# Kernel optimization log

Measured on AMD Instinct MI355X. Metric: run time of the kernel, lower is better.

Reference implementation:

```python
import jax, jax.numpy as jnp
import numpy as np

N = 50000       # nodes
E = 800000      # edges (avg degree 16)
IN_DIM = 64
H = 64          # hidden_dim
OUT_DIM = 64
R = 8           # n_relations
L = 3           # n_layers
LN_EPS = 1e-5
NEG_SLOPE = 0.2


def _layer_norm(x, g, b):
    mu = jnp.mean(x, axis=-1, keepdims=True)
    var = jnp.mean((x - mu) ** 2, axis=-1, keepdims=True)
    return (x - mu) * jax.lax.rsqrt(var + LN_EPS) * g + b


def setup_inputs() -> dict:
    key = jax.random.key(0)
    ks = jax.random.split(key, 10)
    s = 0.05
    return {
        "x": jax.random.normal(ks[0], (N, IN_DIM), jnp.float32),
        "edge_index": jax.random.randint(ks[1], (2, E), 0, N),
        "edge_type": jax.random.randint(ks[2], (E,), 0, R),
        "W_in": jax.random.normal(ks[3], (H, IN_DIM), jnp.float32) * s,
        "b_in": jnp.zeros((H,), jnp.float32),
        "W_rel": jax.random.normal(ks[4], (R, H, H), jnp.float32) * s,   # no bias
        "W_gate": jax.random.normal(ks[5], (R, H, H), jnp.float32) * s,
        "b_gate": jnp.zeros((R, H), jnp.float32),
        "W_att": jax.random.normal(ks[6], (R, 2 * H), jnp.float32) * s,  # Linear(2H,1) per relation
        "b_att": jnp.zeros((R,), jnp.float32),
        "ln_gamma": jnp.ones((L, H), jnp.float32),
        "ln_beta": jnp.zeros((L, H), jnp.float32),
        "W_out": jax.random.normal(ks[7], (OUT_DIM, H), jnp.float32) * s,
        "b_out": jnp.zeros((OUT_DIM,), jnp.float32),
    }


def reference(x, edge_index, edge_type, W_in, b_in, W_rel, W_gate, b_gate,
              W_att, b_att, ln_gamma, ln_beta, W_out, b_out):
    src, dst = edge_index[0], edge_index[1]
    Wa_src, Wa_dst = W_att[:, :H], W_att[:, H:]      # [R,H] each
    seg = dst * R + edge_type                        # combined (node, relation) scatter key
    eidx = jnp.arange(E)

    h = jax.nn.relu(x @ W_in.T + b_in)               # [N,H]

    for layer in range(L):
        h_src = h[src]                               # [E,H] gather
        h_dst = h[dst]                               # [E,H] gather
        # attention score of each edge under its own relation's Linear(2H,1)
        scores_all = h_src @ Wa_src.T + h_dst @ Wa_dst.T + b_att   # [E,R]
        scores = scores_all[eidx, edge_type]                        # [E]
        scores = jax.nn.leaky_relu(scores, NEG_SLOPE)
        # softmax over dim=0 within each relation's edge set (as in the torch code)
        m = jax.ops.segment_max(scores, edge_type, num_segments=R)
        ex = jnp.exp(scores - m[edge_type])
        denom = jax.ops.segment_sum(ex, edge_type, num_segments=R)
        att = ex / denom[edge_type]                                 # [E]
        # relation-specific linear of source features (linear commutes with gather)
        hWr = jnp.einsum('nh,rkh->nrk', h, W_rel)                   # [N,R,H]
        msg = hWr[src, edge_type] * att[:, None]                    # [E,H]
        # per-relation scatter-add into destinations
        agg = jax.ops.segment_sum(msg, seg, num_segments=N * R)     # [N*R,H]
        agg = agg.reshape(N, R, H)
        gate = jax.nn.sigmoid(jnp.einsum('nh,rkh->nrk', h, W_gate) + b_gate)  # [N,R,H]
        h_new = jnp.mean(gate * agg, axis=1)         # sum(messages)/n_relations
        h = jax.nn.relu(_layer_norm(h + h_new, ln_gamma[layer], ln_beta[layer]))

    return h @ W_out.T + b_out
```

## Files before the change

kernel.cpp:

```cpp
#include <hip/hip_runtime.h>
#include <math.h>

#define NN 50000
#define EE 800000
#define HH 64
#define RR 8
#define LL 3
#define NR (NN * RR)
#define NB ((NR + 255) / 256)
#define LN_EPS 1e-5f
#define NEG_SLOPE 0.2f
#define LDH 68
#define OTB (16 * LDH)
#define DSPREAD 64

typedef __attribute__((ext_vector_type(8))) short bf8;
typedef __attribute__((ext_vector_type(4))) float f4;
typedef __attribute__((ext_vector_type(2))) float f2;
typedef __attribute__((ext_vector_type(8))) unsigned short us8;
typedef __attribute__((ext_vector_type(2))) unsigned int u2;
typedef __attribute__((ext_vector_type(4))) unsigned int u4;

#define PIN(x) asm volatile("" :: "v"(x))

#define WLOADP(d0, d1, sbase, vbyte) \
    asm volatile("global_load_dwordx4 %0, %2, %3 offset:0\n\t" \
                 "global_load_dwordx4 %1, %2, %3 offset:64" \
        : "=&v"(d0), "=&v"(d1) : "v"(vbyte), "s"(sbase) : "memory")
#define WWAIT4() do { asm volatile("s_waitcnt vmcnt(4)" ::: "memory"); \
    __builtin_amdgcn_sched_barrier(0); } while (0)
#define WWAIT0() do { asm volatile("s_waitcnt vmcnt(0)" ::: "memory"); \
    __builtin_amdgcn_sched_barrier(0); } while (0)

__device__ __forceinline__ unsigned short bf16r(float f) {
    unsigned u = __float_as_uint(f);
    unsigned r = u + 0x7fffu + ((u >> 16) & 1u);
    return (unsigned short)(r >> 16);
}
__device__ __forceinline__ float bf2f(unsigned short u) {
    return __uint_as_float(((unsigned)u) << 16);
}
__device__ __forceinline__ bf8 asbf8(u4 v) {
    union { u4 a; bf8 b; } c; c.a = v; return c.b;
}
__device__ __forceinline__ void stage16(const void* g, void* l) {
    __builtin_amdgcn_global_load_lds(
        (const __attribute__((address_space(1))) void*)g,
        (__attribute__((address_space(3))) void*)l, 16, 0, 0);
}

__global__ __launch_bounds__(256) void proj_in(
    const float* __restrict__ x, const float* __restrict__ W,
    const float* __restrict__ bias, const unsigned short* __restrict__ WaB,
    float* __restrict__ h, unsigned short* __restrict__ hbf,
    float* __restrict__ s_src, float* __restrict__ s_dst) {
    __shared__ float WT[64 * LDH];
    __shared__ float xs[16 * LDH];
    __shared__ float hs[16 * LDH];
    int tid = threadIdx.x;
    int n0 = blockIdx.x * 16;
    #pragma unroll
    for (int s = 0; s < 16; ++s) {
        int idx = tid + 256 * s;
        int k = idx >> 6, i = idx & 63;
        WT[i * LDH + k] = W[idx];
    }
    int row = tid >> 4, cg = tid & 15;
    {
        f4 v = ((const f4*)x)[(size_t)(n0 + row) * 16 + cg];
        *(f4*)&xs[row * LDH + cg * 4] = v;
    }
    __syncthreads();
    f4 acc;
    {
        f4 b = *(const f4*)(bias + cg * 4);
        acc = b;
        #pragma unroll
        for (int i = 0; i < 64; ++i) {
            float xv = xs[row * LDH + i];
            f4 wt = *(const f4*)&WT[i * LDH + cg * 4];
            acc[0] += xv * wt[0];
            acc[1] += xv * wt[1];
            acc[2] += xv * wt[2];
            acc[3] += xv * wt[3];
        }
        #pragma unroll
        for (int j = 0; j < 4; ++j) acc[j] = fmaxf(acc[j], 0.f);
        int n = n0 + row;
        *(f4*)(h + (size_t)n * 64 + cg * 4) = acc;
        u2 u;
        u[0] = (unsigned)bf16r(acc[0]) | ((unsigned)bf16r(acc[1]) << 16);
        u[1] = (unsigned)bf16r(acc[2]) | ((unsigned)bf16r(acc[3]) << 16);
        *(u2*)(hbf + (size_t)n * 64 + cg * 4) = u;
        *(f4*)&hs[row * LDH + cg * 4] = acc;
    }
    __syncthreads();
    if (tid < 64) {
        int lane = tid;
        int quad = lane >> 4, lr = lane & 15;
        f4 sc = (f4){0.f, 0.f, 0.f, 0.f};
        #pragma unroll
        for (int kb = 0; kb < 2; ++kb) {
            const float* p = &hs[lr * LDH + kb * 32 + quad * 8];
            bf8 a;
            #pragma unroll
            for (int j = 0; j < 8; ++j) a[j] = (short)bf16r(p[j]);
            const bf8* bw = (const bf8*)(WaB + lr * 64 + kb * 32 + quad * 8);
            sc = __builtin_amdgcn_mfma_f32_16x16x32_bf16(a, *bw, sc, 0, 0, 0);
        }
        #pragma unroll
        for (int j = 0; j < 4; ++j) {
            int n = n0 + quad * 4 + j;
            if (lr < 8) s_src[n * 8 + lr] = sc[j];
            else        s_dst[n * 8 + (lr - 8)] = sc[j];
        }
    }
}

__global__ void edge_count(const int* __restrict__ ei, const int* __restrict__ et,
                           int* __restrict__ counts, int* __restrict__ rank) {
    int e = blockIdx.x * 256 + threadIdx.x;
    int d = ei[EE + e], t = et[e];
    rank[e] = atomicAdd(&counts[d * 8 + t], 1);
}

__global__ void scan1(const int* __restrict__ counts, int* __restrict__ offs,
                      int* __restrict__ bsum) {
    __shared__ int s[256];
    int tid = threadIdx.x;
    int i = blockIdx.x * 256 + tid;
    int v = (i < NR) ? counts[i] : 0;
    s[tid] = v; __syncthreads();
    for (int d = 1; d < 256; d <<= 1) {
        int x = (tid >= d) ? s[tid - d] : 0;
        __syncthreads();
        s[tid] += x;
        __syncthreads();
    }
    if (i < NR) offs[i] = s[tid] - v;
    if (tid == 255) bsum[blockIdx.x] = s[255];
}

__global__ void scan2(int* __restrict__ bsum) {
    __shared__ int s[1024];
    int tid = threadIdx.x;
    int carry = 0;
    for (int c0 = 0; c0 < NB; c0 += 1024) {
        int i = c0 + tid;
        int v = (i < NB) ? bsum[i] : 0;
        s[tid] = v; __syncthreads();
        for (int d = 1; d < 1024; d <<= 1) {
            int x = (tid >= d) ? s[tid - d] : 0;
            __syncthreads();
            s[tid] += x;
            __syncthreads();
        }
        if (i < NB) bsum[i] = carry + s[tid] - v;
        int tot = s[1023];
        __syncthreads();
        carry += tot;
    }
}

__global__ void edge_fill(const int* __restrict__ ei, const int* __restrict__ et,
                          const int* __restrict__ rank, const int* __restrict__ offs,
                          const int* __restrict__ bsum, u2* __restrict__ spack) {
    int e = blockIdx.x * 256 + threadIdx.x;
    int s = ei[e], d = ei[EE + e], t = et[e];
    int seg = d * 8 + t;
    int slot = offs[seg] + bsum[seg >> 8] + rank[e];
    spack[slot] = (u2){(unsigned)s, (unsigned)seg};
}

__global__ void cvt_w(const float* __restrict__ Wr, const float* __restrict__ Wg,
                      const float* __restrict__ Wa, const float* __restrict__ Wo,
                      unsigned short* __restrict__ WrB, unsigned short* __restrict__ WgB,
                      unsigned short* __restrict__ WaB, unsigned short* __restrict__ WoB) {
    int i = blockIdx.x * 256 + threadIdx.x;
    WrB[i] = bf16r(Wr[i]);
    WgB[i] = bf16r(Wg[i]);
    if (i < 1024) {
        int row = i >> 6, k = i & 63;
        float v = (row < 8) ? Wa[row * 128 + k] : Wa[(row - 8) * 128 + 64 + k];
        WaB[i] = bf16r(v);
    }
    if (i < 4096) WoB[i] = bf16r(Wo[i]);
}

__global__ void edge_softmax2(const u2* __restrict__ spack,
                              const float* __restrict__ s_src, const float* __restrict__ s_dst,
                              const float* __restrict__ b_att,
                              u2* __restrict__ epack, float* __restrict__ dpart) {
    __shared__ float lsum[4][8];
    int tid = threadIdx.x;
    if (tid < 32) lsum[tid >> 3][tid & 7] = 0.f;
    __syncthreads();
    int slot = blockIdx.x * 256 + tid;
    u2 sp = spack[slot];
    int src = (int)sp[0];
    int seg = (int)sp[1];
    int t = seg & 7;
    float sc = s_src[src * 8 + t] + s_dst[seg] + b_att[t];
    sc = (sc >= 0.f) ? sc : NEG_SLOPE * sc;
    float ex = __expf(sc);
    epack[slot] = (u2){(unsigned)src, __float_as_uint(ex)};
    atomicAdd(&lsum[tid >> 6][t], ex);
    __syncthreads();
    if (tid < 8) {
        float v = lsum[0][tid] + lsum[1][tid] + lsum[2][tid] + lsum[3][tid];
        atomicAdd(&dpart[(blockIdx.x & (DSPREAD - 1)) * 16 + tid], v);
    }
}

__global__ void denom_reduce(const float* __restrict__ dpartL,
                             float* __restrict__ idn8L) {
    __shared__ float sb[256];
    int t = threadIdx.x;
    int rb = t >> 3, ty = t & 7;
    float v = dpartL[rb * 16 + ty] + dpartL[(rb + 32) * 16 + ty];
    sb[t] = v; __syncthreads();
    for (int st = 128; st >= 8; st >>= 1) {
        if (t < st) sb[t] += sb[t + st];
        __syncthreads();
    }
    if (t < 8) idn8L[t] = 1.f / sb[t];
}

__global__ __launch_bounds__(256, 4) void gather_seg(
    const int* __restrict__ offs, const int* __restrict__ bsum,
    const u2* __restrict__ epack, const float* __restrict__ idn8L,
    const unsigned short* __restrict__ hbf_in,
    unsigned short* __restrict__ psG) {
    int tid = threadIdx.x;
    int segl = tid >> 1, half = tid & 1;
    int sidx = blockIdx.x * 128 + segl;
    int lo = offs[sidx] + bsum[sidx >> 8];
    int nxt = sidx + 1;
    int hi = (nxt < NR) ? (offs[nxt] + bsum[nxt >> 8]) : EE;
    int r = segl & 7, gn = segl >> 3;

    f4 d0 = *(const f4*)(idn8L);
    f4 d1 = *(const f4*)(idn8L + 4);
    float i01 = (r & 1) ? d0[1] : d0[0];
    float i23 = (r & 1) ? d0[3] : d0[2];
    float i45 = (r & 1) ? d1[1] : d1[0];
    float i67 = (r & 1) ? d1[3] : d1[2];
    float i03 = (r & 2) ? i23 : i01;
    float i47 = (r & 2) ? i67 : i45;
    float idn = (r & 4) ? i47 : i03;

    f2 acc[16];
    #pragma unroll
    for (int i = 0; i < 16; ++i) acc[i] = (f2){0.f, 0.f};

    for (int s = lo; s < hi; s += 4) {
        int i1 = (s + 1 < hi) ? s + 1 : s;
        int i2 = (s + 2 < hi) ? s + 2 : s;
        int i3 = (s + 3 < hi) ? s + 3 : s;
        u2 pk0 = epack[s], pk1 = epack[i1], pk2 = epack[i2], pk3 = epack[i3];
        float a0 = __uint_as_float(pk0[1]);
        float a1 = (s + 1 < hi) ? __uint_as_float(pk1[1]) : 0.f;
        float a2 = (s + 2 < hi) ? __uint_as_float(pk2[1]) : 0.f;
        float a3 = (s + 3 < hi) ? __uint_as_float(pk3[1]) : 0.f;
        const u4* hp0 = (const u4*)(hbf_in + ((size_t)(int)pk0[0] << 6) + half * 32);
        const u4* hp1 = (const u4*)(hbf_in + ((size_t)(int)pk1[0] << 6) + half * 32);
        const u4* hp2 = (const u4*)(hbf_in + ((size_t)(int)pk2[0] << 6) + half * 32);
        const u4* hp3 = (const u4*)(hbf_in + ((size_t)(int)pk3[0] << 6) + half * 32);
        #pragma unroll
        for (int q = 0; q < 4; ++q) {
            u4 v0 = hp0[q], v1 = hp1[q], v2 = hp2[q], v3 = hp3[q];
            #pragma unroll
            for (int k = 0; k < 4; ++k) {
                f2 w0, w1, w2, w3;
                w0[0] = __uint_as_float(v0[k] << 16);
                w0[1] = __uint_as_float(v0[k] & 0xffff0000u);
                w1[0] = __uint_as_float(v1[k] << 16);
                w1[1] = __uint_as_float(v1[k] & 0xffff0000u);
                w2[0] = __uint_as_float(v2[k] << 16);
                w2[1] = __uint_as_float(v2[k] & 0xffff0000u);
                w3[0] = __uint_as_float(v3[k] << 16);
                w3[1] = __uint_as_float(v3[k] & 0xffff0000u);
                acc[q * 4 + k] += (f2){a0, a0} * w0;
                acc[q * 4 + k] += (f2){a1, a1} * w1;
                acc[q * 4 + k] += (f2){a2, a2} * w2;
                acc[q * 4 + k] += (f2){a3, a3} * w3;
            }
        }
    }

    unsigned short* base = psG + ((size_t)blockIdx.x << 13) + gn * 512 + r * 64;
    #pragma unroll
    for (int q = 0; q < 4; ++q) {
        us8 o;
        #pragma unroll
        for (int k = 0; k < 4; ++k) {
            o[2 * k]     = bf16r(acc[q * 4 + k][0] * idn);
            o[2 * k + 1] = bf16r(acc[q * 4 + k][1] * idn);
        }
        int c2 = (half * 4 + q) ^ (gn & 7);
        *(us8*)(base + c2 * 8) = o;
    }
}

template<bool EMIT, bool OUT>
__global__ __launch_bounds__(256, 4) void combine_dense(
    const float* __restrict__ hbuf, const unsigned short* __restrict__ psG,
    const unsigned short* __restrict__ WrB, const unsigned short* __restrict__ WgB,
    const unsigned short* __restrict__ WaB, const unsigned short* __restrict__ WoB,
    const float* __restrict__ b_gate, const float* __restrict__ gamma,
    const float* __restrict__ beta, float* __restrict__ hout,
    unsigned short* __restrict__ hbf_out, float* __restrict__ ssrc_out,
    float* __restrict__ sdst_out, float* __restrict__ outp,
    const float* __restrict__ b_out) {
    __shared__ unsigned short psL[8192];
    __shared__ float hsL[1024];
    float* ps_f = (float*)psL;
    int tid = threadIdx.x;
    int n0 = blockIdx.x * 16;
    int w = tid >> 6, lane = tid & 63;
    int quad = lane >> 4, lr = lane & 15;
    int tn = w;

    {
        const char* pslice = (const char*)psG + ((size_t)blockIdx.x << 14);
        #pragma unroll
        for (int i = 0; i < 4; ++i) {
            unsigned off = i * 4096 + w * 1024;
            stage16(pslice + off + lane * 16, (char*)psL + off);
        }
        unsigned a = w * 1024 + lane * 16;
        unsigned sa = a ^ (((a >> 8) & 7u) << 4);
        stage16((const char*)(hbuf + (size_t)n0 * 64) + sa, (char*)hsL + a);
    }
    float bgv[8];
    #pragma unroll
    for (int r = 0; r < 8; ++r) bgv[r] = b_gate[r * 64 + tn * 16 + lr];
    #pragma unroll
    for (int r = 0; r < 8; ++r) PIN(bgv[r]);

    __syncthreads();

    unsigned rowb = (unsigned)((tn * 16 + lr) * 128 + quad * 16);
    u4 wr[3][2], wg[3][2];
    WLOADP(wr[0][0], wr[0][1], WrB, rowb);
    WLOADP(wg[0][0], wg[0][1], WgB, rowb);
    WLOADP(wr[1][0], wr[1][1], WrB, rowb + 8192u);
    WLOADP(wg[1][0], wg[1][1], WgB, rowb + 8192u);

    bf8 a_h[2];
    #pragma unroll
    for (int kb = 0; kb < 2; ++kb) {
        unsigned c0 = (unsigned)(kb * 8 + quad * 2)     ^ (unsigned)(lr & 7);
        unsigned c1 = (unsigned)(kb * 8 + quad * 2 + 1) ^ (unsigned)(lr & 7);
        f4 p0 = *(const f4*)((const char*)hsL + lr * 256 + c0 * 16);
        f4 p1 = *(const f4*)((const char*)hsL + lr * 256 + c1 * 16);
        bf8 a;
        #pragma unroll
        for (int j = 0; j < 4; ++j) a[j] = (short)bf16r(p0[j]);
        #pragma unroll
        for (int j = 0; j < 4; ++j) a[4 + j] = (short)bf16r(p1[j]);
        a_h[kb] = a;
    }

    f4 acc = (f4){0.f, 0.f, 0.f, 0.f};
    #pragma unroll
    for (int r = 0; r < 8; ++r) {
        if (r < 7) { WWAIT4(); } else { WWAIT0(); }
        bf8 a_p[2];
        #pragma unroll
        for (int kb = 0; kb < 2; ++kb) {
            unsigned c = (unsigned)(kb * 4 + quad) ^ (unsigned)(lr & 7);
            a_p[kb] = *(const bf8*)((const char*)psL + lr * 1024 + r * 128 + c * 16);
        }
        int rb = r % 3;
        f4 aggc = (f4){0.f, 0.f, 0.f, 0.f};
        f4 gacc = (f4){0.f, 0.f, 0.f, 0.f};
        aggc = __builtin_amdgcn_mfma_f32_16x16x32_bf16(a_p[0], asbf8(wr[rb][0]), aggc, 0, 0, 0);
        gacc = __builtin_amdgcn_mfma_f32_16x16x32_bf16(a_h[0], asbf8(wg[rb][0]), gacc, 0, 0, 0);
        aggc = __builtin_amdgcn_mfma_f32_16x16x32_bf16(a_p[1], asbf8(wr[rb][1]), aggc, 0, 0, 0);
        gacc = __builtin_amdgcn_mfma_f32_16x16x32_bf16(a_h[1], asbf8(wg[rb][1]), gacc, 0, 0, 0);
        if (r + 2 < 8) {
            int nb = (r + 2) % 3;
            unsigned vo = rowb + (unsigned)(r + 2) * 8192u;
            WLOADP(wr[nb][0], wr[nb][1], WrB, vo);
            WLOADP(wg[nb][0], wg[nb][1], WgB, vo);
        }
        #pragma unroll
        for (int j = 0; j < 4; ++j) {
            float g = 1.f / (1.f + __expf(-(gacc[j] + bgv[r])));
            acc[j] += g * aggc[j];
        }
    }
    __syncthreads();

    #pragma unroll
    for (int j = 0; j < 4; ++j) {
        int row = quad * 4 + j;
        int col = tn * 16 + lr;
        unsigned y = (unsigned)(row * 256 + col * 4);
        float hres = *(const float*)((const char*)hsL + (y ^ (((unsigned)(row & 7)) << 4)));
        ps_f[row * LDH + col] = hres + acc[j] * 0.125f;
    }
    __syncthreads();

    {
        int row = tid >> 4, c = tid & 15;
        int n = n0 + row;
        f4 tv = *(const f4*)&ps_f[row * LDH + c * 4];
        float s1 = tv[0] + tv[1] + tv[2] + tv[3];
        float s2 = tv[0]*tv[0] + tv[1]*tv[1] + tv[2]*tv[2] + tv[3]*tv[3];
        #pragma unroll
        for (int off = 1; off <= 8; off <<= 1) {
            s1 += __shfl_xor(s1, off, 64);
            s2 += __shfl_xor(s2, off, 64);
        }
        float mu = s1 * (1.f / 64.f);
        float var = s2 * (1.f / 64.f) - mu * mu;
        float rs = rsqrtf(var + LN_EPS);
        f4 g = *(const f4*)(gamma + c * 4);
        f4 b = *(const f4*)(beta + c * 4);
        f4 ov;
        #pragma unroll
        for (int j = 0; j < 4; ++j)
            ov[j] = fmaxf((tv[j] - mu) * rs * g[j] + b[j], 0.f);
        if (!OUT)
            *(f4*)(hout + (size_t)n * 64 + c * 4) = ov;
        *(f4*)&ps_f[OTB + row * LDH + c * 4] = ov;
        if (EMIT) {
            u2 u;
            u[0] = (unsigned)bf16r(ov[0]) | ((unsigned)bf16r(ov[1]) << 16);
            u[1] = (unsigned)bf16r(ov[2]) | ((unsigned)bf16r(ov[3]) << 16);
            *(u2*)(hbf_out + (size_t)n * 64 + c * 4) = u;
        }
    }

    if (EMIT) {
        __syncthreads();
        if (w == 0) {
            f4 sc = (f4){0.f, 0.f, 0.f, 0.f};
            #pragma unroll
            for (int kb = 0; kb < 2; ++kb) {
                const float* p = &ps_f[OTB + lr * LDH + kb * 32 + quad * 8];
                bf8 a;
                #pragma unroll
                for (int j = 0; j < 8; ++j) a[j] = (short)bf16r(p[j]);
                const bf8* bw = (const bf8*)(WaB + lr * 64 + kb * 32 + quad * 8);
                sc = __builtin_amdgcn_mfma_f32_16x16x32_bf16(a, *bw, sc, 0, 0, 0);
            }
            #pragma unroll
            for (int j = 0; j < 4; ++j) {
                int n = n0 + quad * 4 + j;
                if (lr < 8) ssrc_out[n * 8 + lr] = sc[j];
                else        sdst_out[n * 8 + (lr - 8)] = sc[j];
            }
        }
    }

    if (OUT) {
        __syncthreads();
        f4 oc = (f4){0.f, 0.f, 0.f, 0.f};
        #pragma unroll
        for (int kb = 0; kb < 2; ++kb) {
            const float* p = &ps_f[OTB + lr * LDH + kb * 32 + quad * 8];
            bf8 a;
            #pragma unroll
            for (int j = 0; j < 8; ++j) a[j] = (short)bf16r(p[j]);
            const bf8* bw = (const bf8*)(WoB + ((tn * 16 + lr) * 64 + kb * 32 + quad * 8));
            oc = __builtin_amdgcn_mfma_f32_16x16x32_bf16(a, *bw, oc, 0, 0, 0);
        }
        float bo = b_out[tn * 16 + lr];
        #pragma unroll
        for (int j = 0; j < 4; ++j)
            outp[(size_t)(n0 + quad * 4 + j) * 64 + tn * 16 + lr] = oc[j] + bo;
    }
}

extern "C" void kernel_launch(void* const* d_in, const int* in_sizes, int n_in,
                              void* d_out, int out_size, void* d_ws, size_t ws_size,
                              hipStream_t stream) {
    const float* x      = (const float*)d_in[0];
    const int*   ei     = (const int*)d_in[1];
    const int*   et     = (const int*)d_in[2];
    const float* W_in   = (const float*)d_in[3];
    const float* b_in   = (const float*)d_in[4];
    const float* W_rel  = (const float*)d_in[5];
    const float* W_gate = (const float*)d_in[6];
    const float* b_gate = (const float*)d_in[7];
    const float* W_att  = (const float*)d_in[8];
    const float* b_att  = (const float*)d_in[9];
    const float* ln_g   = (const float*)d_in[10];
    const float* ln_b   = (const float*)d_in[11];
    const float* W_out  = (const float*)d_in[12];
    const float* b_out  = (const float*)d_in[13];
    float* out = (float*)d_out;

    float* h0 = (float*)d_out;

    char* ws = (char*)d_ws;
    float* h1 = (float*)ws;                     ws += (size_t)NN * 64 * 4;
    unsigned short* hbfA = (unsigned short*)ws; ws += (size_t)NN * 64 * 2;
    unsigned short* hbfB = (unsigned short*)ws; ws += (size_t)NN * 64 * 2;
    float* s_src = (float*)ws;                  ws += (size_t)NN * 8 * 4;
    float* s_dst = (float*)ws;                  ws += (size_t)NN * 8 * 4;
    unsigned short* WrB = (unsigned short*)ws;  ws += (size_t)RR * 64 * 64 * 2;
    unsigned short* WgB = (unsigned short*)ws;  ws += (size_t)RR * 64 * 64 * 2;
    unsigned short* WaB = (unsigned short*)ws;  ws += 2048;
    unsigned short* WoB = (unsigned short*)ws;  ws += 8192;
    int* counts = (int*)ws;                     ws += (size_t)NR * 4;
    float* dpart = (float*)ws;                  ws += 3 * DSPREAD * 16 * 4;
    float* idn8G = (float*)ws;                  ws += 3 * 16 * 4;
    int* offs = (int*)ws;                       ws += (size_t)NR * 4;
    int* bsum = (int*)ws;                       ws += 6400;
    int* rank = (int*)ws;                       ws += (size_t)EE * 4;
    u2* spack = (u2*)ws;                        ws += (size_t)EE * 8;
    u2* epack = (u2*)ws;                        ws += (size_t)EE * 8;
    unsigned short* psG = (unsigned short*)ws;  ws += (size_t)NR * 64 * 2;

    hipMemsetAsync(counts, 0, (size_t)NR * 4 + 3 * DSPREAD * 16 * 4, stream);
    cvt_w<<<128, 256, 0, stream>>>(W_rel, W_gate, W_att, W_out, WrB, WgB, WaB, WoB);
    edge_count<<<EE / 256, 256, 0, stream>>>(ei, et, counts, rank);
    scan1<<<NB, 256, 0, stream>>>(counts, offs, bsum);
    scan2<<<1, 1024, 0, stream>>>(bsum);
    edge_fill<<<EE / 256, 256, 0, stream>>>(ei, et, rank, offs, bsum, spack);
    proj_in<<<NN / 16, 256, 0, stream>>>(x, W_in, b_in, WaB, h0, hbfA, s_src, s_dst);

    const int tiles16 = NN / 16;
    float* hA = h0;  float* hB = h1;
    unsigned short* bfA = hbfA;  unsigned short* bfB = hbfB;
    for (int layer = 0; layer < LL; ++layer) {
        float* dpl = dpart + (size_t)layer * DSPREAD * 16;
        float* idn = idn8G + (size_t)layer * 16;
        edge_softmax2<<<EE / 256, 256, 0, stream>>>(spack, s_src, s_dst, b_att,
                                                    epack, dpl);
        denom_reduce<<<1, 256, 0, stream>>>(dpl, idn);
        gather_seg<<<tiles16, 256, 0, stream>>>(offs, bsum, epack, idn, bfA, psG);
        if (layer < LL - 1) {
            combine_dense<true, false><<<tiles16, 256, 0, stream>>>(
                hA, psG, WrB, WgB, WaB, WoB, b_gate,
                ln_g + layer * 64, ln_b + layer * 64,
                hB, bfB, s_src, s_dst, out, b_out);
        } else {
            combine_dense<false, true><<<tiles16, 256, 0, stream>>>(
                hA, psG, WrB, WgB, WaB, WoB, b_gate,
                ln_g + layer * 64, ln_b + layer * 64,
                hB, bfB, s_src, s_dst, out, b_out);
        }
        float* tf = hA; hA = hB; hB = tf;
        unsigned short* tb = bfA; bfA = bfB; bfB = tb;
    }
}
```

Baseline: 460.1 us.

## Make combine_dense persistent over five node tiles with double-buffered LDS staging

Each combine_dense block now processes 80 nodes as five 16-node groups instead of one group. All eight relations' weight fragments are loaded into registers once per block, and the next group's aggregated messages and h rows are staged into a second LDS buffer while the current group computes. This is meant to amortize the weight loads and hide global-to-LDS latency. In exchange, register pressure and LDS use rise (launch bounds drop to 2 blocks per CU), and with only 625 blocks per launch there is less parallelism to spread across the GPU.

```diff
diff --git a/kernel.cpp b/kernel.cpp
--- a/kernel.cpp
+++ b/kernel.cpp
@@ -13,6 +13,8 @@
 #define LDH 68
 #define OTB (16 * LDH)
 #define DSPREAD 64
+#define NPB 80
+#define NGRP 5
 
 typedef __attribute__((ext_vector_type(8))) short bf8;
 typedef __attribute__((ext_vector_type(4))) float f4;
@@ -21,16 +23,10 @@
 typedef __attribute__((ext_vector_type(2))) unsigned int u2;
 typedef __attribute__((ext_vector_type(4))) unsigned int u4;
 
-#define PIN(x) asm volatile("" :: "v"(x))
-
 #define WLOADP(d0, d1, sbase, vbyte) \
     asm volatile("global_load_dwordx4 %0, %2, %3 offset:0\n\t" \
                  "global_load_dwordx4 %1, %2, %3 offset:64" \
         : "=&v"(d0), "=&v"(d1) : "v"(vbyte), "s"(sbase) : "memory")
-#define WWAIT4() do { asm volatile("s_waitcnt vmcnt(4)" ::: "memory"); \
-    __builtin_amdgcn_sched_barrier(0); } while (0)
-#define WWAIT0() do { asm volatile("s_waitcnt vmcnt(0)" ::: "memory"); \
-    __builtin_amdgcn_sched_barrier(0); } while (0)
 
 __device__ __forceinline__ unsigned short bf16r(float f) {
     unsigned u = __float_as_uint(f);
@@ -302,8 +298,21 @@
     }
 }
 
+#define STAGE_GRP(b, g) do { \
+    int n0s_ = nb0 + (g) * 16; \
+    const char* ps_src_ = (const char*)psG + (size_t)n0s_ * 1024; \
+    _Pragma("unroll") \
+    for (int i_ = 0; i_ < 4; ++i_) { \
+        unsigned off_ = i_ * 4096 + w * 1024; \
+        stage16(ps_src_ + off_ + lane * 16, (char*)psL[b] + off_); \
+    } \
+    unsigned a_ = (unsigned)(w * 1024 + lane * 16); \
+    unsigned sa_ = a_ ^ (((a_ >> 8) & 7u) << 4); \
+    stage16((const char*)(hbuf + (size_t)n0s_ * 64) + sa_, (char*)hsL[b] + a_); \
+} while (0)
+
 template<bool EMIT, bool OUT>
-__global__ __launch_bounds__(256, 4) void combine_dense(
+__global__ __launch_bounds__(256, 2) void combine_dense(
     const float* __restrict__ hbuf, const unsigned short* __restrict__ psG,
     const unsigned short* __restrict__ WrB, const unsigned short* __restrict__ WgB,
     const unsigned short* __restrict__ WaB, const unsigned short* __restrict__ WoB,
@@ -312,166 +321,159 @@
     unsigned short* __restrict__ hbf_out, float* __restrict__ ssrc_out,
     float* __restrict__ sdst_out, float* __restrict__ outp,
     const float* __restrict__ b_out) {
-    __shared__ unsigned short psL[8192];
-    __shared__ float hsL[1024];
-    float* ps_f = (float*)psL;
+    __shared__ unsigned short psL[2][8192];
+    __shared__ float hsL[2][1024];
     int tid = threadIdx.x;
-    int n0 = blockIdx.x * 16;
+    int nb0 = blockIdx.x * NPB;
     int w = tid >> 6, lane = tid & 63;
     int quad = lane >> 4, lr = lane & 15;
     int tn = w;
 
-    {
-        const char* pslice = (const char*)psG + ((size_t)blockIdx.x << 14);
-        #pragma unroll
-        for (int i = 0; i < 4; ++i) {
-            unsigned off = i * 4096 + w * 1024;
-            stage16(pslice + off + lane * 16, (char*)psL + off);
-        }
-        unsigned a = w * 1024 + lane * 16;
-        unsigned sa = a ^ (((a >> 8) & 7u) << 4);
-        stage16((const char*)(hbuf + (size_t)n0 * 64) + sa, (char*)hsL + a);
+    STAGE_GRP(0, 0);
+
+    unsigned rowb = (unsigned)((tn * 16 + lr) * 128 + quad * 16);
+    u4 wr[8][2], wg[8][2];
+    #pragma unroll
+    for (int r = 0; r < 8; ++r) {
+        WLOADP(wr[r][0], wr[r][1], WrB, rowb + (unsigned)r * 8192u);
+        WLOADP(wg[r][0], wg[r][1], WgB, rowb + (unsigned)r * 8192u);
     }
     float bgv[8];
     #pragma unroll
     for (int r = 0; r < 8; ++r) bgv[r] = b_gate[r * 64 + tn * 16 + lr];
-    #pragma unroll
-    for (int r = 0; r < 8; ++r) PIN(bgv[r]);
-
-    __syncthreads();
-
-    unsigned rowb = (unsigned)((tn * 16 + lr) * 128 + quad * 16);
-    u4 wr[3][2], wg[3][2];
-    WLOADP(wr[0][0], wr[0][1], WrB, rowb);
-    WLOADP(wg[0][0], wg[0][1], WgB, rowb);
-    WLOADP(wr[1][0], wr[1][1], WrB, rowb + 8192u);
-    WLOADP(wg[1][0], wg[1][1], WgB, rowb + 8192u);
-
-    bf8 a_h[2];
-    #pragma unroll
-    for (int kb = 0; kb < 2; ++kb) {
-        unsigned c0 = (unsigned)(kb * 8 + quad * 2)     ^ (unsigned)(lr & 7);
-        unsigned c1 = (unsigned)(kb * 8 + quad * 2 + 1) ^ (unsigned)(lr & 7);
-        f4 p0 = *(const f4*)((const char*)hsL + lr * 256 + c0 * 16);
-        f4 p1 = *(const f4*)((const char*)hsL + lr * 256 + c1 * 16);
-        bf8 a;
-        #pragma unroll
-        for (int j = 0; j < 4; ++j) a[j] = (short)bf16r(p0[j]);
-        #pragma unroll
-        for (int j = 0; j < 4; ++j) a[4 + j] = (short)bf16r(p1[j]);
-        a_h[kb] = a;
-    }
-
-    f4 acc = (f4){0.f, 0.f, 0.f, 0.f};
-    #pragma unroll
-    for (int r = 0; r < 8; ++r) {
-        if (r < 7) { WWAIT4(); } else { WWAIT0(); }
-        bf8 a_p[2];
+    f4 gmv = *(const f4*)(gamma + (tid & 15) * 4);
+    f4 btv = *(const f4*)(beta + (tid & 15) * 4);
+
+    for (int g = 0; g < NGRP; ++g) {
+        int cb = g & 1;
+        int n0 = nb0 + g * 16;
+        if (g + 1 < NGRP) {
+            STAGE_GRP(cb ^ 1, g + 1);
+            asm volatile("s_waitcnt vmcnt(5)" ::: "memory");
+        } else {
+            asm volatile("s_waitcnt vmcnt(0)" ::: "memory");
+        }
+        __builtin_amdgcn_sched_barrier(0);
+        __builtin_amdgcn_s_barrier();
+
+        bf8 a_h[2];
         #pragma unroll
         for (int kb = 0; kb < 2; ++kb) {
-            unsigned c = (unsigned)(kb * 4 + quad) ^ (unsigned)(lr & 7);
-            a_p[kb] = *(const bf8*)((const char*)psL + lr * 1024 + r * 128 + c * 16);
-        }
-        int rb = r % 3;
-        f4 aggc = (f4){0.f, 0.f, 0.f, 0.f};
-        f4 gacc = (f4){0.f, 0.f, 0.f, 0.f};
-        aggc = __builtin_amdgcn_mfma_f32_16x16x32_bf16(a_p[0], asbf8(wr[rb][0]), aggc, 0, 0, 0);
-        gacc = __builtin_amdgcn_mfma_f32_16x16x32_bf16(a_h[0], asbf8(wg[rb][0]), gacc, 0, 0, 0);
-        aggc = __builtin_amdgcn_mfma_f32_16x16x32_bf16(a_p[1], asbf8(wr[rb][1]), aggc, 0, 0, 0);
-        gacc = __builtin_amdgcn_mfma_f32_16x16x32_bf16(a_h[1], asbf8(wg[rb][1]), gacc, 0, 0, 0);
-        if (r + 2 < 8) {
-            int nb = (r + 2) % 3;
-            unsigned vo = rowb + (unsigned)(r + 2) * 8192u;
-            WLOADP(wr[nb][0], wr[nb][1], WrB, vo);
-            WLOADP(wg[nb][0], wg[nb][1], WgB, vo);
-        }
+            unsigned c0 = (unsigned)(kb * 8 + quad * 2)     ^ (unsigned)(lr & 7);
+            unsigned c1 = (unsigned)(kb * 8 + quad * 2 + 1) ^ (unsigned)(lr & 7);
+            f4 p0 = *(const f4*)((const char*)hsL[cb] + lr * 256 + c0 * 16);
+            f4 p1 = *(const f4*)((const char*)hsL[cb] + lr * 256 + c1 * 16);
+            bf8 a;
+            #pragma unroll
+            for (int j = 0; j < 4; ++j) a[j] = (short)bf16r(p0[j]);
+            #pragma unroll
+            for (int j = 0; j < 4; ++j) a[4 + j] = (short)bf16r(p1[j]);
+            a_h[kb] = a;
+        }
+
+        f4 acc = (f4){0.f, 0.f, 0.f, 0.f};
+        #pragma unroll
+        for (int r = 0; r < 8; ++r) {
+            bf8 a_p[2];
+            #pragma unroll
+            for (int kb = 0; kb < 2; ++kb) {
+                unsigned c = (unsigned)(kb * 4 + quad) ^ (unsigned)(lr & 7);
+                a_p[kb] = *(const bf8*)((const char*)psL[cb] + lr * 1024 + r * 128 + c * 16);
+            }
+            f4 aggc = (f4){0.f, 0.f, 0.f, 0.f};
+            f4 gacc = (f4){0.f, 0.f, 0.f, 0.f};
+            aggc = __builtin_amdgcn_mfma_f32_16x16x32_bf16(a_p[0], asbf8(wr[r][0]), aggc, 0, 0, 0);
+            gacc = __builtin_amdgcn_mfma_f32_16x16x32_bf16(a_h[0], asbf8(wg[r][0]), gacc, 0, 0, 0);
+            aggc = __builtin_amdgcn_mfma_f32_16x16x32_bf16(a_p[1], asbf8(wr[r][1]), aggc, 0, 0, 0);
+            gacc = __builtin_amdgcn_mfma_f32_16x16x32_bf16(a_h[1], asbf8(wg[r][1]), gacc, 0, 0, 0);
+            #pragma unroll
+            for (int j = 0; j < 4; ++j) {
+                float gt = 1.f / (1.f + __expf(-(gacc[j] + bgv[r])));
+                acc[j] += gt * aggc[j];
+            }
+        }
+        __syncthreads();
+
+        float* ps_f = (float*)psL[cb];
         #pragma unroll
         for (int j = 0; j < 4; ++j) {
-            float g = 1.f / (1.f + __expf(-(gacc[j] + bgv[r])));
-            acc[j] += g * aggc[j];
-        }
-    }
-    __syncthreads();
-
-    #pragma unroll
-    for (int j = 0; j < 4; ++j) {
-        int row = quad * 4 + j;
-        int col = tn * 16 + lr;
-        unsigned y = (unsigned)(row * 256 + col * 4);
-        float hres = *(const float*)((const char*)hsL + (y ^ (((unsigned)(row & 7)) << 4)));
-        ps_f[row * LDH + col] = hres + acc[j] * 0.125f;
-    }
-    __syncthreads();
-
-    {
-        int row = tid >> 4, c = tid & 15;
-        int n = n0 + row;
-        f4 tv = *(const f4*)&ps_f[row * LDH + c * 4];
-        float s1 = tv[0] + tv[1] + tv[2] + tv[3];
-        float s2 = tv[0]*tv[0] + tv[1]*tv[1] + tv[2]*tv[2] + tv[3]*tv[3];
-        #pragma unroll
-        for (int off = 1; off <= 8; off <<= 1) {
-            s1 += __shfl_xor(s1, off, 64);
-            s2 += __shfl_xor(s2, off, 64);
-        }
-        float mu = s1 * (1.f / 64.f);
-        float var = s2 * (1.f / 64.f) - mu * mu;
-        float rs = rsqrtf(var + LN_EPS);
-        f4 g = *(const f4*)(gamma + c * 4);
-        f4 b = *(const f4*)(beta + c * 4);
-        f4 ov;
-        #pragma unroll
-        for (int j = 0; j < 4; ++j)
-            ov[j] = fmaxf((tv[j] - mu) * rs * g[j] + b[j], 0.f);
-        if (!OUT)
-            *(f4*)(hout + (size_t)n * 64 + c * 4) = ov;
-        *(f4*)&ps_f[OTB + row * LDH + c * 4] = ov;
+            int row = quad * 4 + j;
+            int col = tn * 16 + lr;
+            unsigned y = (unsigned)(row * 256 + col * 4);
+            float hres = *(const float*)((const char*)hsL[cb] + (y ^ (((unsigned)(row & 7)) << 4)));
+            ps_f[row * LDH + col] = hres + acc[j] * 0.125f;
+        }
+        __syncthreads();
+
+        {
+            int row = tid >> 4, c = tid & 15;
+            int n = n0 + row;
+            f4 tv = *(const f4*)&ps_f[row * LDH + c * 4];
+            float s1 = tv[0] + tv[1] + tv[2] + tv[3];
+            float s2 = tv[0]*tv[0] + tv[1]*tv[1] + tv[2]*tv[2] + tv[3]*tv[3];
+            #pragma unroll
+            for (int off = 1; off <= 8; off <<= 1) {
+                s1 += __shfl_xor(s1, off, 64);
+                s2 += __shfl_xor(s2, off, 64);
+            }
+            float mu = s1 * (1.f / 64.f);
+            float var = s2 * (1.f / 64.f) - mu * mu;
+            float rs = rsqrtf(var + LN_EPS);
+            f4 ov;
+            #pragma unroll
+            for (int j = 0; j < 4; ++j)
+                ov[j] = fmaxf((tv[j] - mu) * rs * gmv[j] + btv[j], 0.f);
+            if (!OUT)
+                *(f4*)(hout + (size_t)n * 64 + c * 4) = ov;
+            *(f4*)&ps_f[OTB + row * LDH + c * 4] = ov;
+            if (EMIT) {
+                u2 u;
+                u[0] = (unsigned)bf16r(ov[0]) | ((unsigned)bf16r(ov[1]) << 16);
+                u[1] = (unsigned)bf16r(ov[2]) | ((unsigned)bf16r(ov[3]) << 16);
+                *(u2*)(hbf_out + (size_t)n * 64 + c * 4) = u;
+            }
+        }
+
         if (EMIT) {
-            u2 u;
-            u[0] = (unsigned)bf16r(ov[0]) | ((unsigned)bf16r(ov[1]) << 16);
-            u[1] = (unsigned)bf16r(ov[2]) | ((unsigned)bf16r(ov[3]) << 16);
-            *(u2*)(hbf_out + (size_t)n * 64 + c * 4) = u;
-        }
-    }
-
-    if (EMIT) {
-        __syncthreads();
-        if (w == 0) {
-            f4 sc = (f4){0.f, 0.f, 0.f, 0.f};
+            __syncthreads();
+            if (w == 0) {
+                f4 sc = (f4){0.f, 0.f, 0.f, 0.f};
+                #pragma unroll
+                for (int kb = 0; kb < 2; ++kb) {
+                    const float* p = &ps_f[OTB + lr * LDH + kb * 32 + quad * 8];
+                    bf8 a;
+                    #pragma unroll
+                    for (int j = 0; j < 8; ++j) a[j] = (short)bf16r(p[j]);
+                    const bf8* bw = (const bf8*)(WaB + lr * 64 + kb * 32 + quad * 8);
+                    sc = __builtin_amdgcn_mfma_f32_16x16x32_bf16(a, *bw, sc, 0, 0, 0);
+                }
+                #pragma unroll
+                for (int j = 0; j < 4; ++j) {
+                    int n = n0 + quad * 4 + j;
+                    if (lr < 8) ssrc_out[n * 8 + lr] = sc[j];
+                    else        sdst_out[n * 8 + (lr - 8)] = sc[j];
+                }
+            }
+        }
+
+        if (OUT) {
+            __syncthreads();
+            f4 oc = (f4){0.f, 0.f, 0.f, 0.f};
             #pragma unroll
             for (int kb = 0; kb < 2; ++kb) {
                 const float* p = &ps_f[OTB + lr * LDH + kb * 32 + quad * 8];
                 bf8 a;
                 #pragma unroll
                 for (int j = 0; j < 8; ++j) a[j] = (short)bf16r(p[j]);
-                const bf8* bw = (const bf8*)(WaB + lr * 64 + kb * 32 + quad * 8);
-                sc = __builtin_amdgcn_mfma_f32_16x16x32_bf16(a, *bw, sc, 0, 0, 0);
-            }
-            #pragma unroll
-            for (int j = 0; j < 4; ++j) {
-                int n = n0 + quad * 4 + j;
-                if (lr < 8) ssrc_out[n * 8 + lr] = sc[j];
-                else        sdst_out[n * 8 + (lr - 8)] = sc[j];
-            }
-        }
-    }
-
-    if (OUT) {
-        __syncthreads();
-        f4 oc = (f4){0.f, 0.f, 0.f, 0.f};
-        #pragma unroll
-        for (int kb = 0; kb < 2; ++kb) {
-            const float* p = &ps_f[OTB + lr * LDH + kb * 32 + quad * 8];
-            bf8 a;
-            #pragma unroll
-            for (int j = 0; j < 8; ++j) a[j] = (short)bf16r(p[j]);
-            const bf8* bw = (const bf8*)(WoB + ((tn * 16 + lr) * 64 + kb * 32 + quad * 8));
-            oc = __builtin_amdgcn_mfma_f32_16x16x32_bf16(a, *bw, oc, 0, 0, 0);
-        }
-        float bo = b_out[tn * 16 + lr];
-        #pragma unroll
-        for (int j = 0; j < 4; ++j)
-            outp[(size_t)(n0 + quad * 4 + j) * 64 + tn * 16 + lr] = oc[j] + bo;
+                const bf8* bw = (const bf8*)(WoB + ((tn * 16 + lr) * 64 + kb * 32 + quad * 8));
+                oc = __builtin_amdgcn_mfma_f32_16x16x32_bf16(a, *bw, oc, 0, 0, 0);
+            }
+            float bo = b_out[tn * 16 + lr];
+            #pragma unroll
+            for (int j = 0; j < 4; ++j)
+                outp[(size_t)(n0 + quad * 4 + j) * 64 + tn * 16 + lr] = oc[j] + bo;
+        }
+        __syncthreads();
     }
 }
 
@@ -525,6 +527,7 @@
     proj_in<<<NN / 16, 256, 0, stream>>>(x, W_in, b_in, WaB, h0, hbfA, s_src, s_dst);
 
     const int tiles16 = NN / 16;
+    const int tiles80 = NN / NPB;
     float* hA = h0;  float* hB = h1;
     unsigned short* bfA = hbfA;  unsigned short* bfB = hbfB;
     for (int layer = 0; layer < LL; ++layer) {
@@ -535,12 +538,12 @@
         denom_reduce<<<1, 256, 0, stream>>>(dpl, idn);
         gather_seg<<<tiles16, 256, 0, stream>>>(offs, bsum, epack, idn, bfA, psG);
         if (layer < LL - 1) {
-            combine_dense<true, false><<<tiles16, 256, 0, stream>>>(
+            combine_dense<true, false><<<tiles80, 256, 0, stream>>>(
                 hA, psG, WrB, WgB, WaB, WoB, b_gate,
                 ln_g + layer * 64, ln_b + layer * 64,
                 hB, bfB, s_src, s_dst, out, b_out);
         } else {
-            combine_dense<false, true><<<tiles16, 256, 0, stream>>>(
+            combine_dense<false, true><<<tiles80, 256, 0, stream>>>(
                 hA, psG, WrB, WgB, WaB, WoB, b_gate,
                 ln_g + layer * 64, ln_b + layer * 64,
                 hB, bfB, s_src, s_dst, out, b_out);
```

Result: faster. 413.5 us (median of 2 runs) (-10.1%).
